# Kernel optimization log

Hardware: AMD Instinct MI355X
Metric: run time of the kernel (lower is better)

Reference implementation:

```python
import jax, jax.numpy as jnp
import numpy as np

BATCH = 128
SITES = 256      # input_dim, number of MPS input cores
BOND = 64        # bond dimension D
FEAT = 2         # feature_dim
OUT = 10         # output_dim


def setup_inputs() -> dict:
    key = jax.random.key(0)
    k1, k2, k3, k4, k5 = jax.random.split(key, 5)
    # forward input: [batch, input_dim, feature_dim], values in [0,1) like a feature map
    input_data = jax.random.uniform(k1, (BATCH, SITES, FEAT), dtype=jnp.float32)
    # InputRegion core tensor, bond_str 'slri' -> [sites, D, D, feat]
    # small random perturbation; identity bias (use_bias=True, fixed_bias) added in forward
    cores = 0.01 * jax.random.normal(k2, (SITES, BOND, BOND, FEAT), dtype=jnp.float32)
    # OutputSite core, bond_str 'olr' -> [output_dim, D, D]
    out_core = 0.01 * jax.random.normal(k3, (OUT, BOND, BOND), dtype=jnp.float32)
    # boundary (edge) vectors for open boundary conditions
    left_vec = jax.random.normal(k4, (BOND,), dtype=jnp.float32) / np.sqrt(BOND)
    right_vec = jax.random.normal(k5, (BOND,), dtype=jnp.float32) / np.sqrt(BOND)
    return {"input_data": input_data, "cores": cores, "out_core": out_core,
            "left_vec": left_vec, "right_vec": right_vec}


def _chain_matmul(mats):
    """Log-depth product of a chain of matrices. mats: [b, s, D, D] -> [b, D, D].
    Product is ordered: mats[:,0] @ mats[:,1] @ ... @ mats[:,s-1]."""
    b, s, d, _ = mats.shape
    while mats.shape[1] > 1:
        n = mats.shape[1]
        if n % 2 == 1:  # pad with identity so length is even
            eye = jnp.broadcast_to(jnp.eye(d, dtype=mats.dtype), (b, 1, d, d))
            mats = jnp.concatenate([mats, eye], axis=1)
        mats = jnp.matmul(mats[:, 0::2], mats[:, 1::2])
    return mats[:, 0]


def reference(input_data, cores, out_core, left_vec, right_vec):
    # InputRegion.forward: contract each core with its per-site feature vector
    # 'slri,bsi->bslr', then add identity bias matrix (use_bias=True)
    mats = jnp.einsum('slri,bsi->bslr', cores, input_data)
    mats = mats + jnp.eye(BOND, dtype=mats.dtype)  # bias_mat = eye, broadcast over b,s

    # split the chain around the (central) output site, reduce each side
    half = SITES // 2
    left_prod = _chain_matmul(mats[:, :half])    # [b, D, D]
    right_prod = _chain_matmul(mats[:, half:])   # [b, D, D]

    # open-boundary contraction: lvec . Lprod . out_core . Rprod . rvec -> [b, out]
    v = jnp.einsum('l,blr->br', left_vec, left_prod)        # [b, D]
    v = jnp.einsum('bl,olr->bor', v, out_core)              # [b, out, D]
    v = jnp.einsum('bol,blr->bor', v, right_prod)           # [b, out, D]
    logits = jnp.einsum('bor,r->bo', v, right_vec)          # [b, out]
    return logits
```

## Files before the change

kernel.cpp:

```cpp
#include <hip/hip_runtime.h>

#define BOND   64
#define SITES  256
#define HALF   128
#define NBATCH 128
#define OUTD   10

#define P1_OFF   1048576
#define VEC_OFF  2097152
#define SITE_F4  2048
#define LPITCH   132

__global__ void __launch_bounds__(256)
mps_pack_kernel(const float* __restrict__ cores, float* __restrict__ P) {
  __shared__ __align__(16) float ld[64 * LPITCH];
  const int s = (int)blockIdx.x;
  const int t = (int)threadIdx.x;
  const float4* src = (const float4*)(cores + (size_t)s * 8192);
  #pragma unroll
  for (int k = 0; k < 8; ++k) {
    const int m = t + 256 * k;
    const int row = m >> 5;
    const int c4  = m & 31;
    *(float4*)&ld[row * LPITCH + c4 * 4] = src[m];
  }
  __syncthreads();
  const bool right = s >= HALF;
  const int step = right ? (SITES - 1 - s) : s;
  float4* out = (float4*)(P + (right ? P1_OFF : 0)) + (size_t)step * SITE_F4;
  #pragma unroll
  for (int k = 0; k < 8; ++k) {
    const int m = t + 256 * k;
    const int g = m >> 6;
    const int j = m & 63;
    float4 v;
    if (!right) {
      const float2 a  = *(const float2*)&ld[(2 * g) * LPITCH + 2 * j];
      const float2 b2 = *(const float2*)&ld[(2 * g + 1) * LPITCH + 2 * j];
      v = make_float4(a.x, a.y, b2.x, b2.y);
    } else {
      v = *(const float4*)&ld[j * LPITCH + 4 * g];
    }
    out[m] = v;
  }
}

__global__ void __launch_bounds__(256, 1)
mps_chain_kernel(const float* __restrict__ input,
                 const float* __restrict__ P,
                 const float* __restrict__ lvec,
                 const float* __restrict__ rvec,
                 float* __restrict__ vout) {
  __shared__ __align__(16) float pa[2][4][BOND][4];
  __shared__ __align__(16) float vshw[4][2][BOND];
  __shared__ __align__(16) float xsh[2][HALF * 2];

  const int t    = (int)threadIdx.x;
  const int w    = t >> 6;
  const int lane = t & 63;
  const int side = (int)blockIdx.x & 1;
  const int pair = (int)blockIdx.x >> 1;
  const int b0   = 2 * pair;
  const int b1   = 2 * pair + 1;

  if (w == 0)
    ((float4*)xsh[0])[lane] =
        ((const float4*)(input + (size_t)b0 * SITES * 2 + side * HALF * 2))[lane];
  else if (w == 1)
    ((float4*)xsh[1])[lane] =
        ((const float4*)(input + (size_t)b1 * SITES * 2 + side * HALF * 2))[lane];

  const float e = side ? rvec[lane] : lvec[lane];
  float vc0 = e, vc1 = e;
  vshw[w][0][lane] = e;
  vshw[w][1][lane] = e;
  float4 v0[4], v1[4];
  #pragma unroll
  for (int qq = 0; qq < 4; ++qq) {
    v0[qq] = ((const float4*)vshw[w][0])[4 * w + qq];
    v1[qq] = ((const float4*)vshw[w][1])[4 * w + qq];
  }

  const float4* base = (const float4*)(P + (side ? P1_OFF : 0)) +
                       (size_t)(8 * w) * 64 + lane;

  float4 A[8], B[8];
  #pragma unroll
  for (int j = 0; j < 8; ++j) A[j] = base[j * 64];

  #define STEP(CUR, NXT, I)                                                  \
  {                                                                          \
    const int inx = ((I) + 1 < HALF) ? (I) + 1 : (I);                        \
    _Pragma("unroll")                                                        \
    for (int j = 0; j < 8; ++j) NXT[j] = base[(size_t)inx * 2048 + j * 64];  \
    float a00 = 0.f, a01 = 0.f, a10 = 0.f, a11 = 0.f;                        \
    _Pragma("unroll")                                                        \
    for (int qq = 0; qq < 4; ++qq) {                                         \
      const float4 m0 = CUR[2 * qq], m1 = CUR[2 * qq + 1];                   \
      const float4 u0 = v0[qq], u1 = v1[qq];                                 \
      a00 = __builtin_fmaf(u0.x, m0.x, a00);                                 \
      a01 = __builtin_fmaf(u0.x, m0.y, a01);                                 \
      a10 = __builtin_fmaf(u1.x, m0.x, a10);                                 \
      a11 = __builtin_fmaf(u1.x, m0.y, a11);                                 \
      a00 = __builtin_fmaf(u0.y, m0.z, a00);                                 \
      a01 = __builtin_fmaf(u0.y, m0.w, a01);                                 \
      a10 = __builtin_fmaf(u1.y, m0.z, a10);                                 \
      a11 = __builtin_fmaf(u1.y, m0.w, a11);                                 \
      a00 = __builtin_fmaf(u0.z, m1.x, a00);                                 \
      a01 = __builtin_fmaf(u0.z, m1.y, a01);                                 \
      a10 = __builtin_fmaf(u1.z, m1.x, a10);                                 \
      a11 = __builtin_fmaf(u1.z, m1.y, a11);                                 \
      a00 = __builtin_fmaf(u0.w, m1.z, a00);                                 \
      a01 = __builtin_fmaf(u0.w, m1.w, a01);                                 \
      a10 = __builtin_fmaf(u1.w, m1.z, a10);                                 \
      a11 = __builtin_fmaf(u1.w, m1.w, a11);                                 \
    }                                                                        \
    *(float4*)pa[(I) & 1][w][lane] = make_float4(a00, a01, a10, a11);        \
    __syncthreads();                                                         \
    const float4 s0 = *(const float4*)pa[(I) & 1][0][lane];                  \
    const float4 s1 = *(const float4*)pa[(I) & 1][1][lane];                  \
    const float4 s2 = *(const float4*)pa[(I) & 1][2][lane];                  \
    const float4 s3 = *(const float4*)pa[(I) & 1][3][lane];                  \
    const float r00 = (s0.x + s1.x) + (s2.x + s3.x);                         \
    const float r01 = (s0.y + s1.y) + (s2.y + s3.y);                         \
    const float r10 = (s0.z + s1.z) + (s2.z + s3.z);                         \
    const float r11 = (s0.w + s1.w) + (s2.w + s3.w);                         \
    const int xi = side ? (HALF - 1 - (I)) : (I);                            \
    const float2 x0 = ((const float2*)xsh[0])[xi];                           \
    const float2 x1 = ((const float2*)xsh[1])[xi];                           \
    vc0 = __builtin_fmaf(x0.x, r00, __builtin_fmaf(x0.y, r01, vc0));         \
    vc1 = __builtin_fmaf(x1.x, r10, __builtin_fmaf(x1.y, r11, vc1));         \
    vshw[w][0][lane] = vc0;                                                  \
    vshw[w][1][lane] = vc1;                                                  \
    _Pragma("unroll")                                                        \
    for (int qq = 0; qq < 4; ++qq) {                                         \
      v0[qq] = ((const float4*)vshw[w][0])[4 * w + qq];                      \
      v1[qq] = ((const float4*)vshw[w][1])[4 * w + qq];                      \
    }                                                                        \
  }

  for (int i = 0; i < HALF; i += 2) {
    STEP(A, B, i);
    STEP(B, A, i + 1);
  }
  #undef STEP

  if (w == 0) {
    vout[((size_t)side * NBATCH + b0) * BOND + lane] = vc0;
    vout[((size_t)side * NBATCH + b1) * BOND + lane] = vc1;
  }
}

__global__ void __launch_bounds__(64)
mps_combine_kernel(const float* __restrict__ oc,
                   const float* __restrict__ vecs,
                   float* __restrict__ out) {
  __shared__ float vl[BOND];
  const int lane = (int)threadIdx.x;
  const int b = (int)blockIdx.x;
  vl[lane] = vecs[b * BOND + lane];
  const float myvr = vecs[NBATCH * BOND + b * BOND + lane];
  float res[OUTD];
  #pragma unroll
  for (int o = 0; o < OUTD; ++o) {
    float acc = 0.f;
    #pragma unroll
    for (int m = 0; m < BOND; ++m)
      acc = __builtin_fmaf(vl[m], oc[((o * BOND) + m) * BOND + lane], acc);
    acc *= myvr;
    #pragma unroll
    for (int off = 32; off > 0; off >>= 1)
      acc += __shfl_xor(acc, off, 64);
    res[o] = acc;
  }
  if (lane == 0) {
    #pragma unroll
    for (int o = 0; o < OUTD; ++o) out[b * OUTD + o] = res[o];
  }
}

extern "C" void kernel_launch(void* const* d_in, const int* in_sizes, int n_in,
                              void* d_out, int out_size, void* d_ws, size_t ws_size,
                              hipStream_t stream) {
  const float* input = (const float*)d_in[0];
  const float* cores = (const float*)d_in[1];
  const float* oc    = (const float*)d_in[2];
  const float* lvec  = (const float*)d_in[3];
  const float* rvec  = (const float*)d_in[4];
  float* ws  = (float*)d_ws;
  float* out = (float*)d_out;

  hipLaunchKernelGGL(mps_pack_kernel, dim3(SITES), dim3(256), 0, stream,
                     cores, ws);
  hipLaunchKernelGGL(mps_chain_kernel, dim3(NBATCH), dim3(256), 0, stream,
                     input, ws, lvec, rvec, ws + VEC_OFF);
  hipLaunchKernelGGL(mps_combine_kernel, dim3(NBATCH), dim3(64), 0, stream,
                     oc, ws + VEC_OFF, out);
}
```

Before: 136.5 us.

## Broadcast chain vector via readlane and apply features before cross-wave reduction

Each wave now broadcasts its 16 vector elements with v_readlane into scalar registers, replacing the per-step LDS write and reload of the running vector. The per-site feature weights are applied to the partial products before they are written to LDS, so only two floats per lane go through the reduction. The full __syncthreads is replaced by an explicit lgkmcnt wait plus a raw s_barrier, and the input features are pre-reversed at load time. This shortens the serial per-step critical path of the 128-step chain, at the cost of 32 readlanes per step and different floating-point summation order.

Result: slower. 146.4 us (+7.2%).

```diff
diff --git a/kernel.cpp b/kernel.cpp
--- a/kernel.cpp
+++ b/kernel.cpp
@@ -45,15 +45,19 @@
   }
 }
 
+__device__ __forceinline__ float rlanef(float v, int l) {
+  return __int_as_float(__builtin_amdgcn_readlane(__float_as_int(v), l));
+}
+
 __global__ void __launch_bounds__(256, 1)
 mps_chain_kernel(const float* __restrict__ input,
                  const float* __restrict__ P,
                  const float* __restrict__ lvec,
                  const float* __restrict__ rvec,
                  float* __restrict__ vout) {
-  __shared__ __align__(16) float pa[2][4][BOND][4];
-  __shared__ __align__(16) float vshw[4][2][BOND];
-  __shared__ __align__(16) float xsh[2][HALF * 2];
+  __shared__ __align__(16) float pa0[2][4][BOND];
+  __shared__ __align__(16) float pa1[2][4][BOND];
+  __shared__ __align__(16) float xsh[2][HALF][2];
 
   const int t    = (int)threadIdx.x;
   const int w    = t >> 6;
@@ -63,22 +67,26 @@
   const int b0   = 2 * pair;
   const int b1   = 2 * pair + 1;
 
-  if (w == 0)
-    ((float4*)xsh[0])[lane] =
-        ((const float4*)(input + (size_t)b0 * SITES * 2 + side * HALF * 2))[lane];
-  else if (w == 1)
-    ((float4*)xsh[1])[lane] =
-        ((const float4*)(input + (size_t)b1 * SITES * 2 + side * HALF * 2))[lane];
+  {
+    const int bi = t >> 7;
+    const int st = t & 127;
+    const int b  = bi ? b1 : b0;
+    const int hs = side ? (HALF - 1 - st) : st;
+    const float2 xv =
+        *(const float2*)(input + ((size_t)b * SITES + side * HALF + hs) * 2);
+    xsh[bi][st][0] = xv.x;
+    xsh[bi][st][1] = xv.y;
+  }
 
   const float e = side ? rvec[lane] : lvec[lane];
-  float vc0 = e, vc1 = e;
-  vshw[w][0][lane] = e;
-  vshw[w][1][lane] = e;
-  float4 v0[4], v1[4];
+  float r0 = e, r1 = e;
+
+  const int wb = 16 * w;
+  float u0[16], u1[16];
   #pragma unroll
-  for (int qq = 0; qq < 4; ++qq) {
-    v0[qq] = ((const float4*)vshw[w][0])[4 * w + qq];
-    v1[qq] = ((const float4*)vshw[w][1])[4 * w + qq];
+  for (int k = 0; k < 16; ++k) {
+    u0[k] = rlanef(r0, wb + k);
+    u1[k] = rlanef(r1, wb + k);
   }
 
   const float4* base = (const float4*)(P + (side ? P1_OFF : 0)) +
@@ -88,54 +96,42 @@
   #pragma unroll
   for (int j = 0; j < 8; ++j) A[j] = base[j * 64];
 
+  __syncthreads();
+
   #define STEP(CUR, NXT, I)                                                  \
   {                                                                          \
     const int inx = ((I) + 1 < HALF) ? (I) + 1 : (I);                        \
     _Pragma("unroll")                                                        \
     for (int j = 0; j < 8; ++j) NXT[j] = base[(size_t)inx * 2048 + j * 64];  \
-    float a00 = 0.f, a01 = 0.f, a10 = 0.f, a11 = 0.f;                        \
+    float p00 = 0.f, p01 = 0.f, p10 = 0.f, p11 = 0.f;                        \
     _Pragma("unroll")                                                        \
-    for (int qq = 0; qq < 4; ++qq) {                                         \
-      const float4 m0 = CUR[2 * qq], m1 = CUR[2 * qq + 1];                   \
-      const float4 u0 = v0[qq], u1 = v1[qq];                                 \
-      a00 = __builtin_fmaf(u0.x, m0.x, a00);                                 \
-      a01 = __builtin_fmaf(u0.x, m0.y, a01);                                 \
-      a10 = __builtin_fmaf(u1.x, m0.x, a10);                                 \
-      a11 = __builtin_fmaf(u1.x, m0.y, a11);                                 \
-      a00 = __builtin_fmaf(u0.y, m0.z, a00);                                 \
-      a01 = __builtin_fmaf(u0.y, m0.w, a01);                                 \
-      a10 = __builtin_fmaf(u1.y, m0.z, a10);                                 \
-      a11 = __builtin_fmaf(u1.y, m0.w, a11);                                 \
-      a00 = __builtin_fmaf(u0.z, m1.x, a00);                                 \
-      a01 = __builtin_fmaf(u0.z, m1.y, a01);                                 \
-      a10 = __builtin_fmaf(u1.z, m1.x, a10);                                 \
-      a11 = __builtin_fmaf(u1.z, m1.y, a11);                                 \
-      a00 = __builtin_fmaf(u0.w, m1.z, a00);                                 \
-      a01 = __builtin_fmaf(u0.w, m1.w, a01);                                 \
-      a10 = __builtin_fmaf(u1.w, m1.z, a10);                                 \
-      a11 = __builtin_fmaf(u1.w, m1.w, a11);                                 \
+    for (int g = 0; g < 8; ++g) {                                            \
+      const float4 m = CUR[g];                                               \
+      p00 = __builtin_fmaf(u0[2 * g], m.x, p00);                             \
+      p01 = __builtin_fmaf(u0[2 * g], m.y, p01);                             \
+      p10 = __builtin_fmaf(u1[2 * g], m.x, p10);                             \
+      p11 = __builtin_fmaf(u1[2 * g], m.y, p11);                             \
+      p00 = __builtin_fmaf(u0[2 * g + 1], m.z, p00);                         \
+      p01 = __builtin_fmaf(u0[2 * g + 1], m.w, p01);                         \
+      p10 = __builtin_fmaf(u1[2 * g + 1], m.z, p10);                         \
+      p11 = __builtin_fmaf(u1[2 * g + 1], m.w, p11);                         \
     }                                                                        \
-    *(float4*)pa[(I) & 1][w][lane] = make_float4(a00, a01, a10, a11);        \
-    __syncthreads();                                                         \
-    const float4 s0 = *(const float4*)pa[(I) & 1][0][lane];                  \
-    const float4 s1 = *(const float4*)pa[(I) & 1][1][lane];                  \
-    const float4 s2 = *(const float4*)pa[(I) & 1][2][lane];                  \
-    const float4 s3 = *(const float4*)pa[(I) & 1][3][lane];                  \
-    const float r00 = (s0.x + s1.x) + (s2.x + s3.x);                         \
-    const float r01 = (s0.y + s1.y) + (s2.y + s3.y);                         \
-    const float r10 = (s0.z + s1.z) + (s2.z + s3.z);                         \
-    const float r11 = (s0.w + s1.w) + (s2.w + s3.w);                         \
-    const int xi = side ? (HALF - 1 - (I)) : (I);                            \
-    const float2 x0 = ((const float2*)xsh[0])[xi];                           \
-    const float2 x1 = ((const float2*)xsh[1])[xi];                           \
-    vc0 = __builtin_fmaf(x0.x, r00, __builtin_fmaf(x0.y, r01, vc0));         \
-    vc1 = __builtin_fmaf(x1.x, r10, __builtin_fmaf(x1.y, r11, vc1));         \
-    vshw[w][0][lane] = vc0;                                                  \
-    vshw[w][1][lane] = vc1;                                                  \
+    const float2 x0 = *(const float2*)xsh[0][(I)];                           \
+    const float2 x1 = *(const float2*)xsh[1][(I)];                           \
+    const float t0 = __builtin_fmaf(x0.x, p00, x0.y * p01);                  \
+    const float t1 = __builtin_fmaf(x1.x, p10, x1.y * p11);                  \
+    pa0[(I) & 1][w][lane] = t0;                                              \
+    pa1[(I) & 1][w][lane] = t1;                                              \
+    asm volatile("s_waitcnt lgkmcnt(0)" ::: "memory");                       \
+    __builtin_amdgcn_s_barrier();                                            \
+    r0 += (pa0[(I) & 1][0][lane] + pa0[(I) & 1][1][lane]) +                  \
+          (pa0[(I) & 1][2][lane] + pa0[(I) & 1][3][lane]);                   \
+    r1 += (pa1[(I) & 1][0][lane] + pa1[(I) & 1][1][lane]) +                  \
+          (pa1[(I) & 1][2][lane] + pa1[(I) & 1][3][lane]);                   \
     _Pragma("unroll")                                                        \
-    for (int qq = 0; qq < 4; ++qq) {                                         \
-      v0[qq] = ((const float4*)vshw[w][0])[4 * w + qq];                      \
-      v1[qq] = ((const float4*)vshw[w][1])[4 * w + qq];                      \
+    for (int k = 0; k < 16; ++k) {                                           \
+      u0[k] = rlanef(r0, wb + k);                                            \
+      u1[k] = rlanef(r1, wb + k);                                            \
     }                                                                        \
   }
 
@@ -146,8 +142,8 @@
   #undef STEP
 
   if (w == 0) {
-    vout[((size_t)side * NBATCH + b0) * BOND + lane] = vc0;
-    vout[((size_t)side * NBATCH + b1) * BOND + lane] = vc1;
+    vout[((size_t)side * NBATCH + b0) * BOND + lane] = r0;
+    vout[((size_t)side * NBATCH + b1) * BOND + lane] = r1;
   }
 }
 
```
